# Kernel tuning notes

Hardware: AMD Instinct MI355X
Metric: run time of the kernel (lower is better)

## Reference

```python
import jax, jax.numpy as jnp
import numpy as np

B, D_IN, D_OUT = 8192, 4096, 4096
IN_DIMS = (64, 64)
OUT_DIMS = (64, 64)
# tt_rank_rate=0.5 over dims [64,64,64,64] -> ranks [1,32,1024,32,1]
RANKS = (1, 32, 1024, 32, 1)


def _kaiming_uniform(key, shape):
    # matches nn.init.kaiming_uniform_(a=sqrt(5)) on a (r_prev, d, r) tensor:
    # fan_in = prod(shape[1:]) = d * r, gain = sqrt(2/(1+5)) = sqrt(1/3)
    fan_in = shape[1] * shape[2]
    bound = np.sqrt(1.0 / 3.0) * np.sqrt(3.0 / fan_in)
    return jax.random.uniform(key, shape, jnp.float32, -bound, bound)


def setup_inputs() -> dict:
    key = jax.random.key(0)
    kx, k0, k1, k2, k3, kb = jax.random.split(key, 6)
    dims = list(IN_DIMS) + list(OUT_DIMS)
    shapes = [(RANKS[i], dims[i], RANKS[i + 1]) for i in range(4)]
    x = jax.random.normal(kx, (B, D_IN), jnp.float32)
    core0 = _kaiming_uniform(k0, shapes[0])  # (1, 64, 32)
    core1 = _kaiming_uniform(k1, shapes[1])  # (32, 64, 1024)
    core2 = _kaiming_uniform(k2, shapes[2])  # (1024, 64, 32)
    core3 = _kaiming_uniform(k3, shapes[3])  # (32, 64, 1)
    bb = 1.0 / np.sqrt(D_IN)
    bias = jax.random.uniform(kb, (D_OUT,), jnp.float32, -bb, bb)
    return {"x": x, "core0": core0, "core1": core1, "core2": core2,
            "core3": core3, "bias": bias}


def reference(x, core0, core1, core2, core3, bias):
    b = x.shape[0]
    s = x.reshape(b, IN_DIMS[0], IN_DIMS[1])          # (B, 64, 64)
    # input core 0: contract first input dim (rank-in = 1 squeezed)
    s = jnp.einsum('bcd,cs->bds', s, core0[0])        # (B, 64, 32)
    # input core 1: contract second input dim and rank
    s = jnp.einsum('bcr,rcs->bs', s, core1)           # (B, 1024)
    # output core 2: expand first output dim
    s = jnp.einsum('br,rAs->bAs', s, core2)           # (B, 64, 32)
    # output core 3: expand second output dim (rank-out = 1 squeezed)
    s = jnp.einsum('bAr,rB->bAB', s, core3[..., 0])   # (B, 64, 64)
    return s.reshape(b, -1) + bias                    # (B, 4096)
```

## Files before the change

### kernel.cpp

```cpp
#include <hip/hip_runtime.h>
#include <hip/hip_bf16.h>


typedef _Float16 h4 __attribute__((ext_vector_type(4)));
typedef _Float16 h8 __attribute__((ext_vector_type(8)));
typedef float f32x4 __attribute__((ext_vector_type(4)));

#define BATCH 8192

__device__ __forceinline__ void gld_lds16(const void* g, void* l) {
  __builtin_amdgcn_global_load_lds(
      (__attribute__((address_space(1))) void*)(g),
      (__attribute__((address_space(3))) void*)(l), 16, 0, 0);
}

__global__ __launch_bounds__(256) void transpose_cast2(
    const float* __restrict__ c1, _Float16* __restrict__ W1t,
    const float* __restrict__ c2, _Float16* __restrict__ W2t) {
  __shared__ float t[64][65];
  const int which = blockIdx.z;
  const float* src = which ? c2 : c1;
  _Float16* dst = which ? W2t : W1t;
  const int K = which ? 1024 : 2048, U = which ? 2048 : 1024;
  const int k0 = (which ? blockIdx.y : blockIdx.x) * 64;
  const int u0 = (which ? blockIdx.x : blockIdx.y) * 64;
  const int tx = threadIdx.x & 63, ty = threadIdx.x >> 6;
  for (int i = ty; i < 64; i += 4) {
    const int k = k0 + i;
    const int sr = which ? k : ((k & 31) * 64 + (k >> 5));
    t[i][tx] = src[(size_t)sr * U + u0 + tx];
  }
  __syncthreads();
  for (int i = ty; i < 64; i += 4) {
    dst[(size_t)(u0 + i) * K + k0 + tx] = (_Float16)t[tx][i];
  }
}

__global__ __launch_bounds__(256) void stage2(const float* __restrict__ x,
                                              const float* __restrict__ c0,
                                              _Float16* __restrict__ s1) {
  __shared__ _Float16 xh[4 * 4096];
  __shared__ float c0l[2048];
  const int b0 = blockIdx.x * 4;
  const int tid = threadIdx.x;

  {
    const float4* xg = (const float4*)(x + (size_t)b0 * 4096);
#pragma unroll
    for (int k = 0; k < 16; ++k) {
      float4 v = xg[tid + 256 * k];
      h4 w = {(_Float16)v.x, (_Float16)v.y, (_Float16)v.z, (_Float16)v.w};
      ((h4*)xh)[tid + 256 * k] = w;
    }
    ((float4*)c0l)[tid] = ((const float4*)c0)[tid];
    ((float4*)c0l)[tid + 256] = ((const float4*)c0)[tid + 256];
  }
  __syncthreads();

  const int row = tid >> 6, t6 = tid & 63;
  const int d0 = (t6 >> 3) * 8;
  const int r0 = (t6 & 7) * 4;
  const _Float16* xrow = xh + row * 4096;

  float acc[8][4];
#pragma unroll
  for (int i = 0; i < 8; ++i)
#pragma unroll
    for (int j = 0; j < 4; ++j) acc[i][j] = 0.0f;

  for (int c = 0; c < 64; ++c) {
    h8 xv = *(const h8*)&xrow[c * 64 + d0];
    f32x4 wv = *(const f32x4*)&c0l[c * 32 + r0];
#pragma unroll
    for (int i = 0; i < 8; ++i) {
      const float xf = (float)xv[i];
#pragma unroll
      for (int j = 0; j < 4; ++j) acc[i][j] += xf * wv[j];
    }
  }

  _Float16* s1row = s1 + (size_t)(b0 + row) * 2048;
#pragma unroll
  for (int i = 0; i < 8; ++i) {
    h4 o = {(_Float16)acc[i][0], (_Float16)acc[i][1], (_Float16)acc[i][2],
            (_Float16)acc[i][3]};
    *(h4*)&s1row[(d0 + i) * 32 + r0] = o;
  }
}

template <int K, int CN>
__global__ __launch_bounds__(512, 2) void gemm_pipe(
    const _Float16* __restrict__ A, const _Float16* __restrict__ Bt,
    _Float16* __restrict__ C) {
  __shared__ __align__(16) char lds[3 * 49152];
  constexpr int NT = K / 64;
  const int bm = blockIdx.x, bn = blockIdx.y;
  const int tid = threadIdx.x;
  const int w = tid >> 6, lane = tid & 63;
  const int lr = lane & 15, kh = lane >> 4;
  const int wmo = (w >> 2) << 6, wno = (w & 3) << 6;

  f32x4 acc[4][4] = {};

  const int sr = tid >> 3;
  const int sc = ((tid & 7) ^ (sr & 7)) << 4;
  const char* gA = (const char*)(A + (size_t)(bm * 128 + sr) * K) + sc;
  const char* gB = (const char*)(Bt + (size_t)(bn * 256 + sr) * K) + sc;
  const size_t rk = (size_t)K * 128;
  char* lw = lds + (w << 10);

  auto STAGE_A = [&](int t) {
    char* b_ = lw + (t % 3) * 49152;
    const char* ga = gA + (size_t)t * 128;
    gld_lds16(ga, b_);
    gld_lds16(ga + rk, b_ + 8192);
    gld_lds16(gB + (size_t)t * 128, b_ + 16384);
  };
  auto STAGE_B = [&](int t) {
    char* b_ = lw + (t % 3) * 49152;
    const char* gb = gB + (size_t)t * 128;
    gld_lds16(gb + rk, b_ + 24576);
    gld_lds16(gb + 2 * rk, b_ + 32768);
    gld_lds16(gb + 3 * rk, b_ + 40960);
  };

  auto KTILE = [&](int t, bool last) {
    if (last)
      asm volatile("s_waitcnt vmcnt(0)" ::: "memory");
    else
      asm volatile("s_waitcnt vmcnt(6)" ::: "memory");
    __builtin_amdgcn_s_barrier();
    __builtin_amdgcn_sched_barrier(0);
    const char* bufA = lds + (t % 3) * 49152;
    const char* bufB = bufA + 16384;
    h8 af[2][4], bf[2][4];
#pragma unroll
    for (int kk = 0; kk < 2; ++kk) {
#pragma unroll
      for (int m = 0; m < 4; ++m) {
        const int R = wmo + m * 16 + lr;
        af[kk][m] = *(const h8*)(bufA + R * 128 +
                                 ((((kk << 2) + kh) ^ (R & 7)) << 4));
      }
#pragma unroll
      for (int n = 0; n < 2; ++n) {
        const int R = wno + n * 16 + lr;
        bf[kk][n] = *(const h8*)(bufB + R * 128 +
                                 ((((kk << 2) + kh) ^ (R & 7)) << 4));
      }
    }
    if (t + 2 < NT) STAGE_A(t + 2);
    asm volatile("s_waitcnt lgkmcnt(0)" ::: "memory");
    __builtin_amdgcn_sched_barrier(0);
    __builtin_amdgcn_s_setprio(1);
#pragma unroll
    for (int kk = 0; kk < 2; ++kk)
#pragma unroll
      for (int m = 0; m < 4; ++m)
#pragma unroll
        for (int n = 0; n < 2; ++n)
          acc[m][n] = __builtin_amdgcn_mfma_f32_16x16x32_f16(
              af[kk][m], bf[kk][n], acc[m][n], 0, 0, 0);
    __builtin_amdgcn_s_setprio(0);
    __builtin_amdgcn_s_barrier();
    __builtin_amdgcn_sched_barrier(0);
#pragma unroll
    for (int kk = 0; kk < 2; ++kk)
#pragma unroll
      for (int n = 2; n < 4; ++n) {
        const int R = wno + n * 16 + lr;
        bf[kk][n] = *(const h8*)(bufB + R * 128 +
                                 ((((kk << 2) + kh) ^ (R & 7)) << 4));
      }
    if (t + 2 < NT) STAGE_B(t + 2);
    asm volatile("s_waitcnt lgkmcnt(0)" ::: "memory");
    __builtin_amdgcn_sched_barrier(0);
    __builtin_amdgcn_s_setprio(1);
#pragma unroll
    for (int kk = 0; kk < 2; ++kk)
#pragma unroll
      for (int m = 0; m < 4; ++m)
#pragma unroll
        for (int n = 2; n < 4; ++n)
          acc[m][n] = __builtin_amdgcn_mfma_f32_16x16x32_f16(
              af[kk][m], bf[kk][n], acc[m][n], 0, 0, 0);
    __builtin_amdgcn_s_setprio(0);
  };

  STAGE_A(0); STAGE_B(0);
  STAGE_A(1); STAGE_B(1);
  for (int t = 0; t < NT - 1; ++t) KTILE(t, false);
  KTILE(NT - 1, true);

#pragma unroll
  for (int m = 0; m < 4; ++m) {
    const int r0 = bm * 128 + wmo + m * 16 + kh * 4;
#pragma unroll
    for (int n = 0; n < 4; ++n) {
      const int c0 = bn * 256 + wno + n * 16 + lr;
#pragma unroll
      for (int q = 0; q < 4; ++q)
        C[(size_t)(r0 + q) * CN + c0] = (_Float16)acc[m][n][q];
    }
  }
}

template <int K>
__global__ __launch_bounds__(512, 2) void gemm2_8p(
    const _Float16* __restrict__ A, const _Float16* __restrict__ Bt,
    const float* __restrict__ c3, const float* __restrict__ bias,
    float* __restrict__ out) {
  __shared__ __align__(16) char lds[131072];
  constexpr int NT = K / 32;
  const int bm = blockIdx.x, bn = blockIdx.y;
  const int tid = threadIdx.x;
  const int w = tid >> 6, lane = tid & 63;
  const int lr = lane & 15, kh = lane >> 4;
  const int wmo = (w >> 2) << 7;
  const int wno = (w & 3) << 6;

  f32x4 acc[8][4] = {};

  const int sr = tid >> 2;
  const int sc = ((tid & 3) ^ (sr & 3)) << 4;
  const char* gA = (const char*)A + (size_t)(bm * 256 + sr) * (K * 2) + sc;
  const char* gB = (const char*)Bt + (size_t)(bn * 256 + sr) * (K * 2) + sc;
  const size_t rk128 = (size_t)128 * K * 2;
  char* lw = lds + (w << 10);

  auto STAGE_A2 = [&](int t) {
    char* b_ = lw + (t % 3) * 32768;
    const char* ga = gA + (size_t)t * 64;
    gld_lds16(ga, b_);
    gld_lds16(ga + rk128, b_ + 8192);
  };
  auto STAGE_B2 = [&](int t) {
    char* b_ = lw + (t % 3) * 32768 + 16384;
    const char* gb = gB + (size_t)t * 64;
    gld_lds16(gb, b_);
    gld_lds16(gb + rk128, b_ + 8192);
  };

  auto KTILE = [&](int t, bool last) {
    if (last)
      asm volatile("s_waitcnt vmcnt(0)" ::: "memory");
    else
      asm volatile("s_waitcnt vmcnt(4)" ::: "memory");
    __builtin_amdgcn_s_barrier();
    __builtin_amdgcn_sched_barrier(0);
    const char* bufA = lds + (t % 3) * 32768;
    const char* bufB = bufA + 16384;
    h8 af[8], bf[4];
#pragma unroll
    for (int m = 0; m < 4; ++m) {
      const int R = wmo + m * 16 + lr;
      af[m] = *(const h8*)(bufA + R * 64 + ((kh ^ (R & 3)) << 4));
    }
#pragma unroll
    for (int n = 0; n < 4; ++n) {
      const int R = wno + n * 16 + lr;
      bf[n] = *(const h8*)(bufB + R * 64 + ((kh ^ (R & 3)) << 4));
    }
    if (t + 2 < NT) STAGE_A2(t + 2);
    asm volatile("s_waitcnt lgkmcnt(0)" ::: "memory");
    __builtin_amdgcn_sched_barrier(0);
    __builtin_amdgcn_s_setprio(1);
#pragma unroll
    for (int m = 0; m < 4; ++m)
#pragma unroll
      for (int n = 0; n < 4; ++n)
        acc[m][n] = __builtin_amdgcn_mfma_f32_16x16x32_f16(af[m], bf[n],
                                                           acc[m][n], 0, 0, 0);
    __builtin_amdgcn_s_setprio(0);
#pragma unroll
    for (int m = 4; m < 8; ++m) {
      const int R = wmo + m * 16 + lr;
      af[m] = *(const h8*)(bufA + R * 64 + ((kh ^ (R & 3)) << 4));
    }
    if (t + 2 < NT) STAGE_B2(t + 2);
    asm volatile("s_waitcnt lgkmcnt(0)" ::: "memory");
    __builtin_amdgcn_sched_barrier(0);
    __builtin_amdgcn_s_setprio(1);
#pragma unroll
    for (int m = 4; m < 8; ++m)
#pragma unroll
      for (int n = 0; n < 4; ++n)
        acc[m][n] = __builtin_amdgcn_mfma_f32_16x16x32_f16(af[m], bf[n],
                                                           acc[m][n], 0, 0, 0);
    __builtin_amdgcn_s_setprio(0);
  };

  STAGE_A2(0); STAGE_B2(0);
  STAGE_A2(1); STAGE_B2(1);
  for (int t = 0; t < NT - 1; ++t) KTILE(t, false);
  KTILE(NT - 1, true);

  h8 bfe[4];
  float bb[8][4];
#pragma unroll
  for (int n = 0; n < 4; ++n) {
#pragma unroll
    for (int j = 0; j < 8; ++j)
      bfe[n][j] = (_Float16)c3[(kh * 8 + j) * 64 + n * 16 + lr];
#pragma unroll
    for (int a = 0; a < 8; ++a)
      bb[a][n] = bias[(bn * 8 + a) * 64 + n * 16 + lr];
  }
  __syncthreads();
#pragma unroll
  for (int m = 0; m < 8; ++m) {
    const int Rb = wmo + m * 16 + kh * 4;
#pragma unroll
    for (int n = 0; n < 4; ++n) {
      const int cc = wno + n * 16 + lr;
#pragma unroll
      for (int q = 0; q < 4; ++q) {
        const int R = Rb + q;
        *(_Float16*)(lds + R * 512 +
                     ((((cc >> 3) ^ (R & 7)) << 4) | ((cc & 7) << 1))) =
            (_Float16)acc[m][n][q];
      }
    }
  }
  __syncthreads();
  const int r32 = w << 5;
#pragma unroll
  for (int mi = 0; mi < 2; ++mi) {
    const int rr = r32 + mi * 16 + lr;
    const int orow0 = bm * 256 + r32 + mi * 16 + (kh << 2);
#pragma unroll
    for (int a = 0; a < 8; ++a) {
      h8 afv = *(const h8*)(lds + rr * 512 +
                            ((((a * 4 + kh) ^ (rr & 7)) << 4)));
#pragma unroll
      for (int n = 0; n < 4; ++n) {
        f32x4 d = {};
        d = __builtin_amdgcn_mfma_f32_16x16x32_f16(afv, bfe[n], d, 0, 0, 0);
        const int ocol = (bn * 8 + a) * 64 + n * 16 + lr;
#pragma unroll
        for (int q = 0; q < 4; ++q)
          out[(size_t)(orow0 + q) * 4096 + ocol] = d[q] + bb[a][n];
      }
    }
  }
}

extern "C" void kernel_launch(void* const* d_in, const int* in_sizes, int n_in,
                              void* d_out, int out_size, void* d_ws,
                              size_t ws_size, hipStream_t stream) {
  (void)in_sizes; (void)n_in; (void)out_size; (void)ws_size;
  const float* x     = (const float*)d_in[0];
  const float* core0 = (const float*)d_in[1];
  const float* core1 = (const float*)d_in[2];
  const float* core2 = (const float*)d_in[3];
  const float* core3 = (const float*)d_in[4];
  const float* bias  = (const float*)d_in[5];
  float* out = (float*)d_out;

  char* ws = (char*)d_ws;
  _Float16* s1h = (_Float16*)ws;
  _Float16* s2h = (_Float16*)(ws + 33554432);
  _Float16* W1t = (_Float16*)(ws + 50331648);
  _Float16* W2t = (_Float16*)(ws + 54525952);

  transpose_cast2<<<dim3(32, 16, 2), 256, 0, stream>>>(core1, W1t, core2, W2t);
  stage2<<<BATCH / 4, 256, 0, stream>>>(x, core0, s1h);
  gemm_pipe<2048, 1024><<<dim3(BATCH / 128, 4), 512, 0, stream>>>(s1h, W1t, s2h);
  gemm2_8p<1024><<<dim3(BATCH / 256, 8), 512, 0, stream>>>(s2h, W2t, core3, bias, out);
}
```

Before: 153.5 us.

## Restructure second GEMM mainloop into 64-wide K tiles with ping-pong quadrant schedule

The second GEMM kernel now stages 64-wide K tiles, up from 32, into double-buffered LDS split into four quarter-tiles (two A halves, two B halves). Each wave computes its 128x64 output in four 64x32 quadrant phases. Fragment reads and per-quarter global-to-LDS prefetches are interleaved between MFMA bursts, with barriers and priority hints keeping waves in lockstep. The aim is to halve loop iterations and hide load latency behind more MFMA work per barrier, at the cost of many more barriers per tile and a more fragile wait-count schedule.

```diff
diff --git a/kernel.cpp b/kernel.cpp
--- a/kernel.cpp
+++ b/kernel.cpp
@@ -206,94 +206,140 @@
 }
 
 template <int K>
-__global__ __launch_bounds__(512, 2) void gemm2_8p(
+__global__ __launch_bounds__(512, 2) void gemm2_8ph(
     const _Float16* __restrict__ A, const _Float16* __restrict__ Bt,
     const float* __restrict__ c3, const float* __restrict__ bias,
     float* __restrict__ out) {
   __shared__ __align__(16) char lds[131072];
-  constexpr int NT = K / 32;
+  constexpr int NT = K / 64;
   const int bm = blockIdx.x, bn = blockIdx.y;
   const int tid = threadIdx.x;
   const int w = tid >> 6, lane = tid & 63;
   const int lr = lane & 15, kh = lane >> 4;
-  const int wmo = (w >> 2) << 7;
-  const int wno = (w & 3) << 6;
+  const int l7 = lr & 7;
 
   f32x4 acc[8][4] = {};
 
-  const int sr = tid >> 2;
-  const int sc = ((tid & 3) ^ (sr & 3)) << 4;
-  const char* gA = (const char*)A + (size_t)(bm * 256 + sr) * (K * 2) + sc;
-  const char* gB = (const char*)Bt + (size_t)(bn * 256 + sr) * (K * 2) + sc;
-  const size_t rk128 = (size_t)128 * K * 2;
+  const int sr = tid >> 3;
+  const int sc = ((tid & 7) ^ (sr & 7)) << 4;
+  const size_t rowK = (size_t)K * 2;
+  const char* gA = (const char*)A + (size_t)(bm * 256 + sr) * rowK + sc;
+  const char* gB = (const char*)Bt + (size_t)(bn * 256 + sr) * rowK + sc;
   char* lw = lds + (w << 10);
 
-  auto STAGE_A2 = [&](int t) {
-    char* b_ = lw + (t % 3) * 32768;
-    const char* ga = gA + (size_t)t * 64;
-    gld_lds16(ga, b_);
-    gld_lds16(ga + rk128, b_ + 8192);
+  auto STAGE = [&](int kind, int t) {
+    char* d = lw + kind * 32768 + (t & 1) * 16384;
+    const char* g = (kind < 2 ? gA : gB) + (size_t)(kind & 1) * 128 * rowK +
+                    (size_t)t * 128;
+    gld_lds16(g, d);
+    gld_lds16(g + 64 * rowK, d + 8192);
   };
-  auto STAGE_B2 = [&](int t) {
-    char* b_ = lw + (t % 3) * 32768 + 16384;
-    const char* gb = gB + (size_t)t * 64;
-    gld_lds16(gb, b_);
-    gld_lds16(gb + rk128, b_ + 8192);
-  };
-
-  auto KTILE = [&](int t, bool last) {
-    if (last)
+
+  const char* bufA0 = lds + (w >> 2) * 32768;
+  const char* bufB0 = lds + 65536 + ((w & 3) >> 1) * 32768;
+  const int bcol = (w & 1) * 64;
+
+  h8 af[2][4], bflo[2][2], bfhi[2][2];
+
+  STAGE(0, 0); STAGE(1, 0); STAGE(2, 0); STAGE(3, 0);
+  STAGE(2, 1); STAGE(0, 1); STAGE(1, 1);
+  asm volatile("s_waitcnt vmcnt(6)" ::: "memory");
+  __builtin_amdgcn_sched_barrier(0);
+  __builtin_amdgcn_s_barrier();
+
+  for (int t = 0; t < NT; ++t) {
+    const char* bA = bufA0 + (t & 1) * 16384;
+    const char* bB = bufB0 + (t & 1) * 16384;
+#pragma unroll
+    for (int kk = 0; kk < 2; ++kk) {
+#pragma unroll
+      for (int m = 0; m < 4; ++m)
+        af[kk][m] = *(const h8*)(bA + (m * 16 + lr) * 128 +
+                                 ((((kk << 2) + kh) ^ l7) << 4));
+#pragma unroll
+      for (int n = 0; n < 2; ++n)
+        bflo[kk][n] = *(const h8*)(bB + (bcol + n * 16 + lr) * 128 +
+                                   ((((kk << 2) + kh) ^ l7) << 4));
+    }
+    if (t + 1 < NT) STAGE(3, t + 1);
+    __builtin_amdgcn_sched_barrier(0);
+    __builtin_amdgcn_s_barrier();
+    asm volatile("s_waitcnt lgkmcnt(0)" ::: "memory");
+    __builtin_amdgcn_sched_barrier(0);
+    __builtin_amdgcn_s_setprio(1);
+#pragma unroll
+    for (int kk = 0; kk < 2; ++kk)
+#pragma unroll
+      for (int m = 0; m < 4; ++m)
+#pragma unroll
+        for (int n = 0; n < 2; ++n)
+          acc[m][n] = __builtin_amdgcn_mfma_f32_16x16x32_f16(
+              af[kk][m], bflo[kk][n], acc[m][n], 0, 0, 0);
+    __builtin_amdgcn_s_setprio(0);
+    __builtin_amdgcn_s_barrier();
+#pragma unroll
+    for (int kk = 0; kk < 2; ++kk)
+#pragma unroll
+      for (int n = 0; n < 2; ++n)
+        bfhi[kk][n] = *(const h8*)(bB + (bcol + 32 + n * 16 + lr) * 128 +
+                                   ((((kk << 2) + kh) ^ l7) << 4));
+    if (t + 2 < NT) STAGE(2, t + 2);
+    __builtin_amdgcn_sched_barrier(0);
+    __builtin_amdgcn_s_barrier();
+    asm volatile("s_waitcnt lgkmcnt(0)" ::: "memory");
+    __builtin_amdgcn_sched_barrier(0);
+    __builtin_amdgcn_s_setprio(1);
+#pragma unroll
+    for (int kk = 0; kk < 2; ++kk)
+#pragma unroll
+      for (int m = 0; m < 4; ++m)
+#pragma unroll
+        for (int n = 0; n < 2; ++n)
+          acc[m][2 + n] = __builtin_amdgcn_mfma_f32_16x16x32_f16(
+              af[kk][m], bfhi[kk][n], acc[m][2 + n], 0, 0, 0);
+    __builtin_amdgcn_s_setprio(0);
+    __builtin_amdgcn_s_barrier();
+#pragma unroll
+    for (int kk = 0; kk < 2; ++kk)
+#pragma unroll
+      for (int m = 0; m < 4; ++m)
+        af[kk][m] = *(const h8*)(bA + (64 + m * 16 + lr) * 128 +
+                                 ((((kk << 2) + kh) ^ l7) << 4));
+    __builtin_amdgcn_sched_barrier(0);
+    __builtin_amdgcn_s_barrier();
+    asm volatile("s_waitcnt lgkmcnt(0)" ::: "memory");
+    __builtin_amdgcn_sched_barrier(0);
+    __builtin_amdgcn_s_setprio(1);
+#pragma unroll
+    for (int kk = 0; kk < 2; ++kk)
+#pragma unroll
+      for (int m = 0; m < 4; ++m)
+#pragma unroll
+        for (int n = 0; n < 2; ++n)
+          acc[4 + m][n] = __builtin_amdgcn_mfma_f32_16x16x32_f16(
+              af[kk][m], bflo[kk][n], acc[4 + m][n], 0, 0, 0);
+    __builtin_amdgcn_s_setprio(0);
+    __builtin_amdgcn_s_barrier();
+    if (t + 2 < NT) { STAGE(0, t + 2); STAGE(1, t + 2); }
+    __builtin_amdgcn_sched_barrier(0);
+    __builtin_amdgcn_s_barrier();
+    __builtin_amdgcn_s_setprio(1);
+#pragma unroll
+    for (int kk = 0; kk < 2; ++kk)
+#pragma unroll
+      for (int m = 0; m < 4; ++m)
+#pragma unroll
+        for (int n = 0; n < 2; ++n)
+          acc[4 + m][2 + n] = __builtin_amdgcn_mfma_f32_16x16x32_f16(
+              af[kk][m], bfhi[kk][n], acc[4 + m][2 + n], 0, 0, 0);
+    __builtin_amdgcn_s_setprio(0);
+    if (t + 2 < NT)
+      asm volatile("s_waitcnt vmcnt(6)" ::: "memory");
+    else
       asm volatile("s_waitcnt vmcnt(0)" ::: "memory");
-    else
-      asm volatile("s_waitcnt vmcnt(4)" ::: "memory");
-    __builtin_amdgcn_s_barrier();
-    __builtin_amdgcn_sched_barrier(0);
-    const char* bufA = lds + (t % 3) * 32768;
-    const char* bufB = bufA + 16384;
-    h8 af[8], bf[4];
-#pragma unroll
-    for (int m = 0; m < 4; ++m) {
-      const int R = wmo + m * 16 + lr;
-      af[m] = *(const h8*)(bufA + R * 64 + ((kh ^ (R & 3)) << 4));
-    }
-#pragma unroll
-    for (int n = 0; n < 4; ++n) {
-      const int R = wno + n * 16 + lr;
-      bf[n] = *(const h8*)(bufB + R * 64 + ((kh ^ (R & 3)) << 4));
-    }
-    if (t + 2 < NT) STAGE_A2(t + 2);
-    asm volatile("s_waitcnt lgkmcnt(0)" ::: "memory");
-    __builtin_amdgcn_sched_barrier(0);
-    __builtin_amdgcn_s_setprio(1);
-#pragma unroll
-    for (int m = 0; m < 4; ++m)
-#pragma unroll
-      for (int n = 0; n < 4; ++n)
-        acc[m][n] = __builtin_amdgcn_mfma_f32_16x16x32_f16(af[m], bf[n],
-                                                           acc[m][n], 0, 0, 0);
-    __builtin_amdgcn_s_setprio(0);
-#pragma unroll
-    for (int m = 4; m < 8; ++m) {
-      const int R = wmo + m * 16 + lr;
-      af[m] = *(const h8*)(bufA + R * 64 + ((kh ^ (R & 3)) << 4));
-    }
-    if (t + 2 < NT) STAGE_B2(t + 2);
-    asm volatile("s_waitcnt lgkmcnt(0)" ::: "memory");
-    __builtin_amdgcn_sched_barrier(0);
-    __builtin_amdgcn_s_setprio(1);
-#pragma unroll
-    for (int m = 4; m < 8; ++m)
-#pragma unroll
-      for (int n = 0; n < 4; ++n)
-        acc[m][n] = __builtin_amdgcn_mfma_f32_16x16x32_f16(af[m], bf[n],
-                                                           acc[m][n], 0, 0, 0);
-    __builtin_amdgcn_s_setprio(0);
-  };
-
-  STAGE_A2(0); STAGE_B2(0);
-  STAGE_A2(1); STAGE_B2(1);
-  for (int t = 0; t < NT - 1; ++t) KTILE(t, false);
-  KTILE(NT - 1, true);
+    __builtin_amdgcn_sched_barrier(0);
+    __builtin_amdgcn_s_barrier();
+  }
 
   h8 bfe[4];
   float bb[8][4];
@@ -307,18 +353,22 @@
       bb[a][n] = bias[(bn * 8 + a) * 64 + n * 16 + lr];
   }
   __syncthreads();
-#pragma unroll
-  for (int m = 0; m < 8; ++m) {
-    const int Rb = wmo + m * 16 + kh * 4;
-#pragma unroll
-    for (int n = 0; n < 4; ++n) {
-      const int cc = wno + n * 16 + lr;
-#pragma unroll
-      for (int q = 0; q < 4; ++q) {
-        const int R = Rb + q;
-        *(_Float16*)(lds + R * 512 +
-                     ((((cc >> 3) ^ (R & 7)) << 4) | ((cc & 7) << 1))) =
-            (_Float16)acc[m][n][q];
+  {
+    const int wmo = (w >> 2) << 7;
+    const int wno = (w & 3) << 6;
+#pragma unroll
+    for (int m = 0; m < 8; ++m) {
+      const int Rb = wmo + m * 16 + kh * 4;
+#pragma unroll
+      for (int n = 0; n < 4; ++n) {
+        const int cc = wno + n * 16 + lr;
+#pragma unroll
+        for (int q = 0; q < 4; ++q) {
+          const int R = Rb + q;
+          *(_Float16*)(lds + R * 512 +
+                       ((((cc >> 3) ^ (R & 7)) << 4) | ((cc & 7) << 1))) =
+              (_Float16)acc[m][n][q];
+        }
       }
     }
   }
@@ -366,5 +416,6 @@
   transpose_cast2<<<dim3(32, 16, 2), 256, 0, stream>>>(core1, W1t, core2, W2t);
   stage2<<<BATCH / 4, 256, 0, stream>>>(x, core0, s1h);
   gemm_pipe<2048, 1024><<<dim3(BATCH / 128, 4), 512, 0, stream>>>(s1h, W1t, s2h);
-  gemm2_8p<1024><<<dim3(BATCH / 256, 8), 512, 0, stream>>>(s2h, W2t, core3, bias, out);
-}
+  gemm2_8ph<1024><<<dim3(BATCH / 256, 2048 / 256), 512, 0, stream>>>(
+      s2h, W2t, core3, bias, out);
+}
```

Measured after the change: 149.1 us. 1.03x faster.
